# Kernel tuning notes

Measured on AMD Instinct MI355X. Metric: run time of the kernel, lower is better.

The kernel has to match this reference:

```python
import jax, jax.numpy as jnp
import numpy as np

LN_EPS = 1e-5
SUM_CLAMP = 1e-12


def setup_inputs() -> dict:
    key = jax.random.key(0)
    ks = jax.random.split(key, 10)
    L, D, H, P, E = 200000, 512, 512, 16384, 200000
    lesion_x = jax.random.normal(ks[0], (L, D), dtype=jnp.float32)
    edge_index = jnp.stack([
        jax.random.randint(ks[1], (E,), 0, P),   # patient idx
        jax.random.randint(ks[2], (E,), 0, L),   # lesion idx
    ], axis=0).astype(jnp.int64)
    s1 = 1.0 / np.sqrt(D)
    s2 = 1.0 / np.sqrt(H)
    W1 = jax.random.uniform(ks[3], (H, D), jnp.float32, -s1, s1)
    b1 = jax.random.uniform(ks[4], (H,), jnp.float32, -s1, s1)
    W2 = jax.random.uniform(ks[5], (1, H), jnp.float32, -s2, s2)
    b2 = jax.random.uniform(ks[6], (1,), jnp.float32, -s2, s2)
    Wp = jax.random.uniform(ks[7], (768, D), jnp.float32, -s1, s1)
    bp = jax.random.uniform(ks[8], (768,), jnp.float32, -s1, s1)
    gamma = jnp.ones((768,), jnp.float32)
    beta = jnp.zeros((768,), jnp.float32)
    return dict(lesion_x=lesion_x, patient_to_lesion_edge_index=edge_index,
                num_patients_in_batch=P, W1=W1, b1=b1, W2=W2, b2=b2,
                Wp=Wp, bp=bp, gamma=gamma, beta=beta)


def reference(lesion_x, patient_to_lesion_edge_index, num_patients_in_batch,
              W1, b1, W2, b2, Wp, bp, gamma, beta):
    P = int(num_patients_in_batch)
    pat = patient_to_lesion_edge_index[0]
    les = patient_to_lesion_edge_index[1]
    feats = lesion_x[les]                                  # [E, D] gather
    h = jnp.tanh(feats @ W1.T + b1)                        # [E, H]
    scores = (h @ W2.T + b2)[:, 0]                         # [E]
    smax = jax.ops.segment_max(scores, pat, num_segments=P)  # [P]
    ex = jnp.exp(scores - smax[pat])                       # [E]
    esum = jax.ops.segment_sum(ex, pat, num_segments=P)
    esum = jnp.maximum(esum, SUM_CLAMP)
    alpha = ex / esum[pat]                                 # [E]
    agg = jax.ops.segment_sum(feats * alpha[:, None], pat, num_segments=P)  # [P, D]
    proj = agg @ Wp.T + bp                                 # [P, 768]
    mu = jnp.mean(proj, axis=-1, keepdims=True)
    var = jnp.mean(jnp.square(proj - mu), axis=-1, keepdims=True)
    out = (proj - mu) * jax.lax.rsqrt(var + LN_EPS) * gamma + beta
    return out
```

## Files before the change

### kernel.cpp

```cpp
#include <hip/hip_runtime.h>
#include <hip/hip_bf16.h>

#define D_DIM 512
#define H_DIM 512
#define O_DIM 768

using bf16x8 = __attribute__((ext_vector_type(8))) short;
using f32x4  = __attribute__((ext_vector_type(4))) float;

static __device__ __forceinline__ unsigned cvtpk(float lo, float hi){
  unsigned r;
  asm("v_cvt_pk_bf16_f32 %0, %1, %2" : "=v"(r) : "v"(lo), "v"(hi));
  return r;
}

static __device__ __forceinline__ float bflo(unsigned u){
  return __uint_as_float(u << 16);
}
static __device__ __forceinline__ float bfhi(unsigned u){
  return __uint_as_float(u & 0xffff0000u);
}

static __device__ __forceinline__ float fast_tanh(float x){
  float e = __expf(2.f * x);
  return 1.f - 2.f / (e + 1.f);
}

static __device__ __forceinline__ unsigned f2ord(float f){
  unsigned u = __float_as_uint(f);
  return (u & 0x80000000u) ? ~u : (u | 0x80000000u);
}
static __device__ __forceinline__ float ord2f(unsigned u){
  u = (u & 0x80000000u) ? (u & 0x7fffffffu) : ~u;
  return __uint_as_float(u);
}

static __device__ __forceinline__ void gload16(const void* g, void* l){
  __builtin_amdgcn_global_load_lds(
      (const __attribute__((address_space(1))) void*)g,
      (__attribute__((address_space(3))) void*)l, 16, 0, 0);
}

__global__ void cvt_bf16(const float* __restrict__ in,
                         unsigned short* __restrict__ out, int n8)
{
  int stride = gridDim.x * blockDim.x;
  for (int i = blockIdx.x*blockDim.x + threadIdx.x; i < n8; i += stride){
    const float4* p = (const float4*)in + (size_t)i*2;
    float4 a = p[0], b = p[1];
    uint4 pk;
    pk.x = cvtpk(a.x, a.y);
    pk.y = cvtpk(a.z, a.w);
    pk.z = cvtpk(b.x, b.y);
    pk.w = cvtpk(b.z, b.w);
    ((uint4*)out)[i] = pk;
  }
}

__launch_bounds__(256, 4)
__global__ void gemm1_hc(const float* __restrict__ A,
                         const short* __restrict__ Bm,
                         const float* __restrict__ bias,
                         const float* __restrict__ w2,
                         float* __restrict__ out,
                         short* __restrict__ Ab,
                         int M, int nwg)
{
  __shared__ short lds_a[128*32];
  __shared__ short lds_b[128*32];

  const int q  = nwg >> 3, rr = nwg & 7;
  const int xcd = blockIdx.x & 7, bidx = blockIdx.x >> 3;
  const int swz = (xcd < rr ? xcd*(q+1) : rr*(q+1) + (xcd-rr)*q) + bidx;
  const int colBase = (swz & 3) * 128;
  const int rowBase = (swz >> 2) * 128;
  const bool writeAb = (colBase == 0);

  const int tid  = threadIdx.x;
  const int lane = tid & 63;
  const int w    = tid >> 6;
  const int wr   = w >> 1, wc = w & 1;
  const int lr   = lane & 15;
  const int lk   = lane >> 4;

  const int arow = tid >> 3;
  const int af4  = tid & 7;
  const int rlocB = lane >> 2;
  const int jB    = lane & 3;

  f32x4 acc[4][4];
  #pragma unroll
  for (int i = 0; i < 4; ++i)
    #pragma unroll
    for (int j = 0; j < 4; ++j)
      acc[i][j] = (f32x4){0.f, 0.f, 0.f, 0.f};

  for (int kt = 0; kt < 16; ++kt){
    const int kOff = kt * 32;
    float4 va[4];
    #pragma unroll
    for (int c = 0; c < 4; ++c){
      int gA = rowBase + c*32 + arow; if (gA > M-1) gA = M-1;
      va[c] = *(const float4*)(A + (size_t)gA*512 + kOff + af4*4);
    }
    #pragma unroll
    for (int c = 0; c < 2; ++c){
      int rt = w*32 + c*16 + rlocB;
      int js = jB ^ ((rt >> 1) & 3);
      gload16(Bm + (size_t)(colBase + rt)*512 + kOff + js*8,
              &lds_b[(w*32 + c*16)*32]);
    }
    #pragma unroll
    for (int c = 0; c < 4; ++c){
      int rt = c*32 + arow;
      uint2 pk = { cvtpk(va[c].x, va[c].y), cvtpk(va[c].z, va[c].w) };
      int g  = (af4 >> 1) ^ ((rt >> 1) & 3);
      int si = rt*32 + g*8 + (af4 & 1)*4;
      *(uint2*)&lds_a[si] = pk;
      if (writeAb){
        int gA = rowBase + rt;
        if (gA < M) *(uint2*)(Ab + (size_t)gA*512 + kOff + af4*4) = pk;
      }
    }
    __syncthreads();
    bf16x8 af[4], bfr[4];
    #pragma unroll
    for (int mf = 0; mf < 4; ++mf){
      int r  = wr*64 + mf*16 + lr;
      int g  = lk ^ ((r >> 1) & 3);
      af[mf] = *(bf16x8*)&lds_a[r*32 + g*8];
    }
    #pragma unroll
    for (int nf = 0; nf < 4; ++nf){
      int r  = wc*64 + nf*16 + lr;
      int g  = lk ^ ((r >> 1) & 3);
      bfr[nf] = *(bf16x8*)&lds_b[r*32 + g*8];
    }
    #pragma unroll
    for (int mf = 0; mf < 4; ++mf)
      #pragma unroll
      for (int nf = 0; nf < 4; ++nf)
        acc[mf][nf] = __builtin_amdgcn_mfma_f32_16x16x32_bf16(
            af[mf], bfr[nf], acc[mf][nf], 0, 0, 0);
    __syncthreads();
  }

  #pragma unroll
  for (int mf = 0; mf < 4; ++mf){
    float part[4] = {0.f,0.f,0.f,0.f};
    #pragma unroll
    for (int nf = 0; nf < 4; ++nf){
      int gc = colBase + wc*64 + nf*16 + lr;
      float b = bias[gc], wv = w2[gc];
      #pragma unroll
      for (int r = 0; r < 4; ++r)
        part[r] += fast_tanh(acc[mf][nf][r] + b) * wv;
    }
    #pragma unroll
    for (int r = 0; r < 4; ++r){
      part[r] += __shfl_xor(part[r], 1);
      part[r] += __shfl_xor(part[r], 2);
      part[r] += __shfl_xor(part[r], 4);
      part[r] += __shfl_xor(part[r], 8);
    }
    if (lr == 0){
      int gr = rowBase + wr*64 + mf*16 + lk*4;
      #pragma unroll
      for (int r = 0; r < 4; ++r)
        if (gr + r < M) atomicAdd(&out[gr + r], part[r]);
    }
  }
}

__launch_bounds__(512, 1)
__global__ void gemm2_ln(const short* __restrict__ A,
                         const short* __restrict__ Bm,
                         const float* __restrict__ bp,
                         const float* __restrict__ gamma,
                         const float* __restrict__ beta,
                         float* __restrict__ out)
{
  __shared__ short lds_a[64*64];
  __shared__ short lds_b[768*64];
  __shared__ float redS[64*8];
  __shared__ float redQ[64*8];
  __shared__ float muArr[64];
  __shared__ float invArr[64];

  const int tid  = threadIdx.x;
  const int lane = tid & 63;
  const int w    = tid >> 6;
  const int lr   = lane & 15;
  const int lk   = lane >> 4;
  const int rowBase = blockIdx.x * 64;
  const int rloc = lane >> 3;
  const int jg   = lane & 7;

  f32x4 acc[4][6];
  #pragma unroll
  for (int i = 0; i < 4; ++i)
    #pragma unroll
    for (int j = 0; j < 6; ++j)
      acc[i][j] = (f32x4){0.f, 0.f, 0.f, 0.f};

  for (int kt = 0; kt < 8; ++kt){
    const int kOff = kt * 64;
    {
      int rt = w*8 + rloc;
      int js = jg ^ (rt & 7);
      gload16(A + (size_t)(rowBase + rt)*512 + kOff + js*8, &lds_a[(w*8)*64]);
    }
    #pragma unroll
    for (int c = 0; c < 12; ++c){
      int rt = w*96 + c*8 + rloc;
      int js = jg ^ (rt & 7);
      gload16(Bm + (size_t)rt*512 + kOff + js*8, &lds_b[(w*96 + c*8)*64]);
    }
    __syncthreads();
    #pragma unroll
    for (int kk = 0; kk < 2; ++kk){
      bf16x8 af[4], bfr[6];
      #pragma unroll
      for (int mf = 0; mf < 4; ++mf){
        int r   = mf*16 + lr;
        int idx = (r*64 + kk*32 + lk*8) ^ ((r & 7) << 3);
        af[mf] = *(bf16x8*)&lds_a[idx];
      }
      #pragma unroll
      for (int nf = 0; nf < 6; ++nf){
        int r   = w*96 + nf*16 + lr;
        int idx = (r*64 + kk*32 + lk*8) ^ ((r & 7) << 3);
        bfr[nf] = *(bf16x8*)&lds_b[idx];
      }
      __builtin_amdgcn_s_setprio(1);
      #pragma unroll
      for (int mf = 0; mf < 4; ++mf)
        #pragma unroll
        for (int nf = 0; nf < 6; ++nf)
          acc[mf][nf] = __builtin_amdgcn_mfma_f32_16x16x32_bf16(
              af[mf], bfr[nf], acc[mf][nf], 0, 0, 0);
      __builtin_amdgcn_s_setprio(0);
    }
    __syncthreads();
  }

  float s1[4][4], s2[4][4];
  #pragma unroll
  for (int mf = 0; mf < 4; ++mf)
    #pragma unroll
    for (int r = 0; r < 4; ++r){ s1[mf][r] = 0.f; s2[mf][r] = 0.f; }
  #pragma unroll
  for (int mf = 0; mf < 4; ++mf)
    #pragma unroll
    for (int nf = 0; nf < 6; ++nf){
      int gc = w*96 + nf*16 + lr;
      float b = bp[gc];
      #pragma unroll
      for (int r = 0; r < 4; ++r){
        float v = acc[mf][nf][r] + b;
        s1[mf][r] += v;
        s2[mf][r] += v*v;
      }
    }
  #pragma unroll
  for (int mf = 0; mf < 4; ++mf)
    #pragma unroll
    for (int r = 0; r < 4; ++r){
      #pragma unroll
      for (int d = 1; d < 16; d <<= 1){
        s1[mf][r] += __shfl_xor(s1[mf][r], d);
        s2[mf][r] += __shfl_xor(s2[mf][r], d);
      }
    }
  if (lr == 0){
    #pragma unroll
    for (int mf = 0; mf < 4; ++mf)
      #pragma unroll
      for (int r = 0; r < 4; ++r){
        int row = mf*16 + lk*4 + r;
        redS[row*8 + w] = s1[mf][r];
        redQ[row*8 + w] = s2[mf][r];
      }
  }
  __syncthreads();
  if (tid < 64){
    float s = 0.f, qq = 0.f;
    #pragma unroll
    for (int j = 0; j < 8; ++j){ s += redS[tid*8 + j]; qq += redQ[tid*8 + j]; }
    float mu  = s * (1.f/768.f);
    float var = qq * (1.f/768.f) - mu*mu;
    muArr[tid]  = mu;
    invArr[tid] = rsqrtf(var + 1e-5f);
  }
  __syncthreads();

  #pragma unroll
  for (int mf = 0; mf < 4; ++mf)
    #pragma unroll
    for (int nf = 0; nf < 6; ++nf){
      int gc = w*96 + nf*16 + lr;
      float b = bp[gc], g = gamma[gc], be = beta[gc];
      #pragma unroll
      for (int r = 0; r < 4; ++r){
        int row = mf*16 + lk*4 + r;
        float v = acc[mf][nf][r] + b;
        out[(size_t)(rowBase + row)*768 + gc] =
            (v - muArr[row]) * invArr[row] * g + be;
      }
    }
}

__global__ void edge_pass1(const int* __restrict__ edge, int E,
                           const float* __restrict__ scores,
                           unsigned* __restrict__ smax_o,
                           int* __restrict__ hist)
{
  int e = blockIdx.x*256 + threadIdx.x;
  if (e >= E) return;
  int p = edge[e], l = edge[E + e];
  atomicMax(&smax_o[p], f2ord(scores[l]));
  atomicAdd(&hist[p], 1);
}

__global__ void scan_kernel(const int* __restrict__ hist,
                            int* __restrict__ offsets, int P)
{
  __shared__ int s[1024];
  int t = threadIdx.x;
  int local[16]; int sum = 0;
  #pragma unroll
  for (int i = 0; i < 16; ++i){
    int idx = t*16 + i;
    local[i] = (idx < P) ? hist[idx] : 0;
    sum += local[i];
  }
  s[t] = sum;
  __syncthreads();
  for (int off = 1; off < 1024; off <<= 1){
    int v = (t >= off) ? s[t - off] : 0;
    __syncthreads();
    s[t] += v;
    __syncthreads();
  }
  int run = s[t] - sum;
  #pragma unroll
  for (int i = 0; i < 16; ++i){
    int idx = t*16 + i;
    if (idx < P) offsets[idx] = run;
    run += local[i];
  }
}

__global__ void edge_pass2(const int* __restrict__ edge, int E,
                           const float* __restrict__ scores,
                           const unsigned* __restrict__ smax_o,
                           float* __restrict__ ex,
                           float* __restrict__ esum,
                           const int* __restrict__ offsets,
                           int* __restrict__ cursor,
                           int* __restrict__ sorted)
{
  int e = blockIdx.x*256 + threadIdx.x;
  if (e >= E) return;
  int p = edge[e], l = edge[E + e];
  float v = __expf(scores[l] - ord2f(smax_o[p]));
  ex[e] = v;
  atomicAdd(&esum[p], v);
  int pos = atomicAdd(&cursor[p], 1);
  sorted[offsets[p] + pos] = e;
}

__global__ void agg_kernel(const int* __restrict__ edge, int E,
                           const short* __restrict__ Ab,
                           const float* __restrict__ ex,
                           const float* __restrict__ esum,
                           const int* __restrict__ offsets,
                           const int* __restrict__ hist,
                           const int* __restrict__ sorted,
                           unsigned* __restrict__ aggb)
{
  int p    = blockIdx.x*4 + (threadIdx.x >> 6);
  int lane = threadIdx.x & 63;
  int n = hist[p];
  if (n == 0) return;
  int start = offsets[p];
  float inv = 1.f / fmaxf(esum[p], 1e-12f);
  float a[8] = {0.f,0.f,0.f,0.f,0.f,0.f,0.f,0.f};
  int e0 = sorted[start];
  uint4 u = *(const uint4*)(Ab + (size_t)edge[E + e0]*512 + lane*8);
  float alpha = ex[e0] * inv;
  for (int i = 0; i < n; ++i){
    uint4 uc = u; float ac = alpha;
    if (i + 1 < n){
      int e2 = sorted[start + i + 1];
      u = *(const uint4*)(Ab + (size_t)edge[E + e2]*512 + lane*8);
      alpha = ex[e2] * inv;
    }
    a[0] += ac * bflo(uc.x);  a[1] += ac * bfhi(uc.x);
    a[2] += ac * bflo(uc.y);  a[3] += ac * bfhi(uc.y);
    a[4] += ac * bflo(uc.z);  a[5] += ac * bfhi(uc.z);
    a[6] += ac * bflo(uc.w);  a[7] += ac * bfhi(uc.w);
  }
  uint4 o = { cvtpk(a[0],a[1]), cvtpk(a[2],a[3]),
              cvtpk(a[4],a[5]), cvtpk(a[6],a[7]) };
  *(uint4*)&aggb[(size_t)p*256 + lane*4] = o;
}

extern "C" void kernel_launch(void* const* d_in, const int* in_sizes, int n_in,
                              void* d_out, int out_size, void* d_ws, size_t ws_size,
                              hipStream_t stream)
{
  const float* lesion_x = (const float*)d_in[0];
  const int*   edge     = (const int*)d_in[1];
  const float* W1    = (const float*)d_in[3];
  const float* b1    = (const float*)d_in[4];
  const float* W2    = (const float*)d_in[5];
  const float* Wp    = (const float*)d_in[7];
  const float* bp    = (const float*)d_in[8];
  const float* gamma = (const float*)d_in[9];
  const float* beta  = (const float*)d_in[10];

  const int L = in_sizes[0] / D_DIM;
  const int E = in_sizes[1] / 2;
  const int P = out_size / O_DIM;

  auto al = [](size_t x){ return (x + 255) & ~(size_t)255; };
  char* ws = (char*)d_ws;
  size_t oScores = 0;
  size_t oSmax   = oScores + al((size_t)L*4);
  size_t oEsum   = oSmax   + al((size_t)P*4);
  size_t oHist   = oEsum   + al((size_t)P*4);
  size_t oCursor = oHist   + al((size_t)P*4);
  size_t smallEnd= oCursor + al((size_t)P*4);
  size_t oAggB   = smallEnd;
  size_t aggEnd  = oAggB   + al((size_t)P*D_DIM*2);
  size_t oOff    = aggEnd;
  size_t oEx     = oOff    + al((size_t)P*4);
  size_t oSorted = oEx     + al((size_t)E*4);
  size_t oW1b    = oSorted + al((size_t)E*4);
  size_t oWpb    = oW1b    + al((size_t)H_DIM*D_DIM*2);
  size_t oAb     = oWpb    + al((size_t)O_DIM*D_DIM*2);
  size_t need    = oAb     + al((size_t)L*D_DIM*2);
  (void)need;

  float*    scores = (float*)(ws + oScores);
  unsigned* smax_o = (unsigned*)(ws + oSmax);
  float*    esum   = (float*)(ws + oEsum);
  int*      hist   = (int*)(ws + oHist);
  int*      cursor = (int*)(ws + oCursor);
  unsigned* aggb   = (unsigned*)(ws + oAggB);
  int*      offs   = (int*)(ws + oOff);
  float*    ex     = (float*)(ws + oEx);
  int*      sorted = (int*)(ws + oSorted);
  short*    W1b    = (short*)(ws + oW1b);
  short*    Wpb    = (short*)(ws + oWpb);
  short*    Ab     = (short*)(ws + oAb);

  hipMemsetAsync(d_ws, 0, smallEnd, stream);
  hipMemsetAsync(ws + oAggB, 0, (size_t)P*D_DIM*2, stream);

  dim3 b256(256);
  int eb = (E + 255) / 256;

  cvt_bf16<<<128, b256, 0, stream>>>(W1, (unsigned short*)W1b, H_DIM*D_DIM/8);
  cvt_bf16<<<192, b256, 0, stream>>>(Wp, (unsigned short*)Wpb, O_DIM*D_DIM/8);

  int nRow = (L + 127) / 128;
  int nwg  = 4 * nRow;
  gemm1_hc<<<nwg, b256, 0, stream>>>(lesion_x, W1b, b1, W2, scores, Ab, L, nwg);

  edge_pass1<<<eb, b256, 0, stream>>>(edge, E, scores, smax_o, hist);
  scan_kernel<<<1, 1024, 0, stream>>>(hist, offs, P);
  edge_pass2<<<eb, b256, 0, stream>>>(edge, E, scores, smax_o, ex, esum,
                                      offs, cursor, sorted);
  agg_kernel<<<P/4, b256, 0, stream>>>(edge, E, Ab, ex, esum, offs,
                                       hist, sorted, aggb);
  gemm2_ln<<<P/64, dim3(512), 0, stream>>>((const short*)aggb, Wpb, bp,
                                           gamma, beta, (float*)d_out);
}
```

Baseline: 428.6 us.

## Load GEMM1 operands directly into registers, dropping the LDS staging

The first GEMM now loads A (fp32, converted to bf16 in registers) and W1 (bf16) straight from global memory into MFMA fragment registers. This removes the shared-memory tiles and the two barriers per K step, and the K loop is fully unrolled. In exchange, global loads are duplicated across waves: each A row is read by both column waves and each W1 row by both row waves. The loads are also less coalesced (16-byte chunks per lane across rows), and launch bounds drop to 2 blocks per SM for the extra register pressure.

```diff
diff --git a/kernel.cpp b/kernel.cpp
--- a/kernel.cpp
+++ b/kernel.cpp
@@ -57,24 +57,20 @@
   }
 }
 
-__launch_bounds__(256, 4)
-__global__ void gemm1_hc(const float* __restrict__ A,
-                         const short* __restrict__ Bm,
-                         const float* __restrict__ bias,
-                         const float* __restrict__ w2,
-                         float* __restrict__ out,
-                         short* __restrict__ Ab,
-                         int M, int nwg)
-{
-  __shared__ short lds_a[128*32];
-  __shared__ short lds_b[128*32];
-
+__launch_bounds__(256, 2)
+__global__ void gemm1_reg(const float* __restrict__ A,
+                          const short* __restrict__ Bm,
+                          const float* __restrict__ bias,
+                          const float* __restrict__ w2,
+                          float* __restrict__ out,
+                          short* __restrict__ Ab,
+                          int M, int nwg)
+{
   const int q  = nwg >> 3, rr = nwg & 7;
   const int xcd = blockIdx.x & 7, bidx = blockIdx.x >> 3;
   const int swz = (xcd < rr ? xcd*(q+1) : rr*(q+1) + (xcd-rr)*q) + bidx;
   const int colBase = (swz & 3) * 128;
   const int rowBase = (swz >> 2) * 128;
-  const bool writeAb = (colBase == 0);
 
   const int tid  = threadIdx.x;
   const int lane = tid & 63;
@@ -82,11 +78,23 @@
   const int wr   = w >> 1, wc = w & 1;
   const int lr   = lane & 15;
   const int lk   = lane >> 4;
-
-  const int arow = tid >> 3;
-  const int af4  = tid & 7;
-  const int rlocB = lane >> 2;
-  const int jB    = lane & 3;
+  const bool writeAb = (colBase == 0) && (wc == 0);
+
+  const float* pa[4];
+  short*       pab[4];
+  #pragma unroll
+  for (int mf = 0; mf < 4; ++mf){
+    int r = rowBase + wr*64 + mf*16 + lr;
+    if (r > M-1) r = M-1;
+    pa[mf]  = A  + (size_t)r*512 + lk*8;
+    pab[mf] = Ab + (size_t)r*512 + lk*8;
+  }
+  const short* pb[4];
+  #pragma unroll
+  for (int nf = 0; nf < 4; ++nf){
+    int c = colBase + wc*64 + nf*16 + lr;
+    pb[nf] = Bm + (size_t)c*512 + lk*8;
+  }
 
   f32x4 acc[4][4];
   #pragma unroll
@@ -95,54 +103,35 @@
     for (int j = 0; j < 4; ++j)
       acc[i][j] = (f32x4){0.f, 0.f, 0.f, 0.f};
 
-  for (int kt = 0; kt < 16; ++kt){
-    const int kOff = kt * 32;
-    float4 va[4];
-    #pragma unroll
-    for (int c = 0; c < 4; ++c){
-      int gA = rowBase + c*32 + arow; if (gA > M-1) gA = M-1;
-      va[c] = *(const float4*)(A + (size_t)gA*512 + kOff + af4*4);
-    }
-    #pragma unroll
-    for (int c = 0; c < 2; ++c){
-      int rt = w*32 + c*16 + rlocB;
-      int js = jB ^ ((rt >> 1) & 3);
-      gload16(Bm + (size_t)(colBase + rt)*512 + kOff + js*8,
-              &lds_b[(w*32 + c*16)*32]);
-    }
-    #pragma unroll
-    for (int c = 0; c < 4; ++c){
-      int rt = c*32 + arow;
-      uint2 pk = { cvtpk(va[c].x, va[c].y), cvtpk(va[c].z, va[c].w) };
-      int g  = (af4 >> 1) ^ ((rt >> 1) & 3);
-      int si = rt*32 + g*8 + (af4 & 1)*4;
-      *(uint2*)&lds_a[si] = pk;
-      if (writeAb){
-        int gA = rowBase + rt;
-        if (gA < M) *(uint2*)(Ab + (size_t)gA*512 + kOff + af4*4) = pk;
-      }
-    }
-    __syncthreads();
-    bf16x8 af[4], bfr[4];
-    #pragma unroll
-    for (int mf = 0; mf < 4; ++mf){
-      int r  = wr*64 + mf*16 + lr;
-      int g  = lk ^ ((r >> 1) & 3);
-      af[mf] = *(bf16x8*)&lds_a[r*32 + g*8];
-    }
-    #pragma unroll
-    for (int nf = 0; nf < 4; ++nf){
-      int r  = wc*64 + nf*16 + lr;
-      int g  = lk ^ ((r >> 1) & 3);
-      bfr[nf] = *(bf16x8*)&lds_b[r*32 + g*8];
-    }
-    #pragma unroll
-    for (int mf = 0; mf < 4; ++mf)
+  #pragma unroll
+  for (int kt = 0; kt < 8; ++kt){
+    #pragma unroll
+    for (int kk = 0; kk < 2; ++kk){
+      const int ko = kt*64 + kk*32;
+      bf16x8 bfr[4];
       #pragma unroll
       for (int nf = 0; nf < 4; ++nf)
-        acc[mf][nf] = __builtin_amdgcn_mfma_f32_16x16x32_bf16(
-            af[mf], bfr[nf], acc[mf][nf], 0, 0, 0);
-    __syncthreads();
+        bfr[nf] = *(const bf16x8*)(pb[nf] + ko);
+      bf16x8 af[4];
+      #pragma unroll
+      for (int mf = 0; mf < 4; ++mf){
+        float4 lo = *(const float4*)(pa[mf] + ko);
+        float4 hi = *(const float4*)(pa[mf] + ko + 4);
+        union { bf16x8 v; unsigned u[4]; } fa;
+        fa.u[0] = cvtpk(lo.x, lo.y);
+        fa.u[1] = cvtpk(lo.z, lo.w);
+        fa.u[2] = cvtpk(hi.x, hi.y);
+        fa.u[3] = cvtpk(hi.z, hi.w);
+        af[mf] = fa.v;
+        if (writeAb) *(bf16x8*)(pab[mf] + ko) = fa.v;
+      }
+      #pragma unroll
+      for (int mf = 0; mf < 4; ++mf)
+        #pragma unroll
+        for (int nf = 0; nf < 4; ++nf)
+          acc[mf][nf] = __builtin_amdgcn_mfma_f32_16x16x32_bf16(
+              af[mf], bfr[nf], acc[mf][nf], 0, 0, 0);
+    }
   }
 
   #pragma unroll
@@ -467,7 +456,7 @@
 
   int nRow = (L + 127) / 128;
   int nwg  = 4 * nRow;
-  gemm1_hc<<<nwg, b256, 0, stream>>>(lesion_x, W1b, b1, W2, scores, Ab, L, nwg);
+  gemm1_reg<<<nwg, b256, 0, stream>>>(lesion_x, W1b, b1, W2, scores, Ab, L, nwg);
 
   edge_pass1<<<eb, b256, 0, stream>>>(edge, E, scores, smax_o, hist);
   scan_kernel<<<1, 1024, 0, stream>>>(hist, offs, P);
```

Measured after the change: 779.8 us. 81.9% more time.
